# Kernel tuning notes

Hardware: AMD Instinct MI355X
Metric: run time of the kernel (lower is better)

## Reference

```python
import jax, jax.numpy as jnp
import numpy as np

NUM_STATES = 32768
NUM_LABELS = 64
BATCH = 512


def setup_inputs() -> dict:
    key = jax.random.key(0)
    k1, k2, k3, k4 = jax.random.split(key, 4)
    f = jax.random.normal(k1, (BATCH, NUM_LABELS), dtype=jnp.float32)
    # legal_state: binary indicator matrix [num_states, num_labels]
    S = jax.random.randint(k2, (NUM_STATES, NUM_LABELS), 0, 2).astype(jnp.float32)
    y = jax.random.uniform(k3, (BATCH, NUM_LABELS), dtype=jnp.float32)
    mask = jax.random.randint(k4, (BATCH, NUM_LABELS), 0, 2).astype(jnp.float32)
    return {"f": f, "S": S, "y": y, "mask": mask}


def reference(f, S, y, mask):
    # potential[s, b] = sum_i S[s, i] * f[b, i]
    potential = jnp.einsum('si,bi->sb', S, f)
    # stable softmax over the state axis (replaces exp/max/sum in original)
    P = jax.nn.softmax(potential, axis=0)  # [num_states, batch]
    # pMargin[b, i] = sum_{s: S[s,i]>0} P[s, b]  ->  indicator-matrix GEMM
    pMargin = jnp.einsum('sb,si->bi', P, S)  # [batch, num_labels]
    # per-column BCE (torch BCELoss clamps log at -100), masked, mean over batch
    logp = jnp.clip(jnp.log(pMargin), -100.0, None)
    log1mp = jnp.clip(jnp.log(1.0 - pMargin), -100.0, None)
    bce = -(y * logp + (1.0 - y) * log1mp) * mask  # [batch, num_labels]
    loss = jnp.sum(jnp.mean(bce, axis=0))  # sum over columns of per-column means
    return loss, pMargin
```

## Files before the change

kernel.cpp:

```cpp
#include <hip/hip_runtime.h>
#include <hip/hip_bf16.h>
#include <math.h>

#define N_STATES 32768
#define N_LABELS 64
#define N_BATCH  512

#define WS_M_F   0
#define ZP_F     1024
#define UP_F     65536
#define SB_BYTE  8650752u
#define STB_BYTE 12845056u

typedef __attribute__((ext_vector_type(8))) short          bfrag;
typedef __attribute__((ext_vector_type(4))) float          f32x4;
typedef __attribute__((ext_vector_type(8))) unsigned short u16x8;

static __device__ __forceinline__ unsigned short f2bf(float x) {
    __hip_bfloat16 h = __float2bfloat16(x);
    return *reinterpret_cast<unsigned short*>(&h);
}
static __device__ __forceinline__ float bf2f(unsigned short u) {
    __hip_bfloat16 h;
    *reinterpret_cast<unsigned short*>(&h) = u;
    return __bfloat162float(h);
}

typedef __attribute__((address_space(1))) const unsigned char g_u8;
typedef __attribute__((address_space(3))) unsigned char       l_u8;
static __device__ __forceinline__ void dma16(const void* g, void* l) {
    __builtin_amdgcn_global_load_lds((g_u8*)g, (l_u8*)l, 16, 0, 0);
}

__global__ __launch_bounds__(256) void prep_kernel(
    const float* __restrict__ f, const float* __restrict__ S,
    float* __restrict__ ws) {
    const int tb = blockIdx.x;
    const int t  = threadIdx.x;

    if (tb == 512) {
        for (int b = t; b < N_BATCH; b += 256) {
            const float* fr = f + b * N_LABELS;
            float m = 0.f;
            #pragma unroll
            for (int i = 0; i < N_LABELS; i++) m += fmaxf(fr[i], 0.f);
            ws[WS_M_F + b] = m;
        }
        return;
    }

    __shared__ alignas(16) unsigned short Sl[64 * 72];

    unsigned short* SbW = (unsigned short*)((char*)ws + SB_BYTE);
    unsigned short* StW = (unsigned short*)((char*)ws + STB_BYTE);

    const int r = t >> 2;
    const int q = t & 3;
    const int m = r & 7;

    const float4* p4 = reinterpret_cast<const float4*>(
        S + ((size_t)(tb * 64 + r)) * N_LABELS + q * 16);
    float4 v0 = p4[0], v1 = p4[1], v2 = p4[2], v3 = p4[3];
    float vf[16] = {v0.x,v0.y,v0.z,v0.w, v1.x,v1.y,v1.z,v1.w,
                    v2.x,v2.y,v2.z,v2.w, v3.x,v3.y,v3.z,v3.w};
    u16x8 lo8, hi8;
    #pragma unroll
    for (int j = 0; j < 8; j++) { lo8[j] = f2bf(vf[j]); hi8[j] = f2bf(vf[8 + j]); }

    *(u16x8*)&Sl[r * 72 + q * 16]     = lo8;
    *(u16x8*)&Sl[r * 72 + q * 16 + 8] = hi8;

    {
        unsigned short* dst = SbW + (size_t)tb * 4096 + r * 64 + (((2 * q) ^ (m & 6)) * 8);
        if (m & 1) { *(u16x8*)dst = hi8; *(u16x8*)(dst + 8) = lo8; }
        else       { *(u16x8*)dst = lo8; *(u16x8*)(dst + 8) = hi8; }
    }
    __syncthreads();

    const int i  = r;
    const int mi = i & 7;
    u16x8 tlo, thi;
    #pragma unroll
    for (int j = 0; j < 8; j++) {
        tlo[j] = Sl[(16 * q + j)     * 72 + i];
        thi[j] = Sl[(16 * q + 8 + j) * 72 + i];
    }
    {
        unsigned short* dst = StW + (size_t)tb * 4096 + i * 64 + (((2 * q) ^ (mi & 6)) * 8);
        if (mi & 1) { *(u16x8*)dst = thi; *(u16x8*)(dst + 8) = tlo; }
        else        { *(u16x8*)dst = tlo; *(u16x8*)(dst + 8) = thi; }
    }
}

__global__ __launch_bounds__(256, 2) void fused_kernel(
    const float* __restrict__ f, float* __restrict__ ws,
    float* __restrict__ out) {
    __shared__ alignas(16) unsigned short Sb2[2][4096];
    __shared__ alignas(16) unsigned short St2[2][4096];
    __shared__ alignas(16) unsigned short Et[64 * 72];

    const float* M = ws + WS_M_F;
    const char* SbG = (const char*)ws + SB_BYTE;
    const char* StG = (const char*)ws + STB_BYTE;

    const int t     = threadIdx.x;
    const int lane  = t & 63;
    const int w     = t >> 6;
    const int x     = lane & 15;
    const int quad  = lane >> 4;
    const int mm    = x & 7;
    const int btile = blockIdx.x >> 6;
    const int chunk = blockIdx.x & 63;
    const int tile0 = chunk * 8;

    bfrag fh[4][2], fl[4][2];
    #pragma unroll
    for (int nt = 0; nt < 4; nt++) {
        const float4* fp = reinterpret_cast<const float4*>(
            f + ((size_t)(btile * 64 + nt * 16 + x)) * N_LABELS);
        #pragma unroll
        for (int kh = 0; kh < 2; kh++) {
            float4 a = fp[kh * 8 + quad * 2];
            float4 b = fp[kh * 8 + quad * 2 + 1];
            float vv[8] = {a.x,a.y,a.z,a.w, b.x,b.y,b.z,b.w};
            #pragma unroll
            for (int j = 0; j < 8; j++) {
                unsigned short h = f2bf(vv[j]);
                fh[nt][kh][j] = (short)h;
                fl[nt][kh][j] = (short)f2bf(vv[j] - bf2f(h));
            }
        }
    }
    float Mv[4];
    #pragma unroll
    for (int nt = 0; nt < 4; nt++) Mv[nt] = M[btile * 64 + nt * 16 + x];

    f32x4 Uacc[4];
    #pragma unroll
    for (int nt = 0; nt < 4; nt++) Uacc[nt] = (f32x4){0.f, 0.f, 0.f, 0.f};
    float zacc[4] = {0.f, 0.f, 0.f, 0.f};

    auto stage = [&](int tile, int buf) {
        size_t gb = (size_t)tile * 8192 + (size_t)w * 2048 + (size_t)lane * 16;
        int lo = w * 2048;
        dma16(SbG + gb,        (char*)&Sb2[buf][0] + lo);
        dma16(SbG + gb + 1024, (char*)&Sb2[buf][0] + lo + 1024);
        dma16(StG + gb,        (char*)&St2[buf][0] + lo);
        dma16(StG + gb + 1024, (char*)&St2[buf][0] + lo + 1024);
    };

    stage(tile0 + 0, 0);
    stage(tile0 + 1, 1);
    asm volatile("s_waitcnt vmcnt(4)" ::: "memory");
    asm volatile("s_barrier" ::: "memory");

    #pragma unroll
    for (int st = 0; st < 8; st++) {
        const int cur = st & 1;
        const unsigned short* Sb = &Sb2[cur][0];
        const unsigned short* St = &St2[cur][0];

        bfrag a0 = *(const bfrag*)(Sb + (16 * w + x) * 64 + ((quad ^ mm) * 8));
        bfrag a1 = *(const bfrag*)(Sb + (16 * w + x) * 64 + (((quad + 4) ^ mm) * 8));
        #pragma unroll
        for (int nt = 0; nt < 4; nt++) {
            f32x4 acc = (f32x4){0.f, 0.f, 0.f, 0.f};
            acc = __builtin_amdgcn_mfma_f32_16x16x32_bf16(a0, fh[nt][0], acc, 0, 0, 0);
            acc = __builtin_amdgcn_mfma_f32_16x16x32_bf16(a1, fh[nt][1], acc, 0, 0, 0);
            acc = __builtin_amdgcn_mfma_f32_16x16x32_bf16(a0, fl[nt][0], acc, 0, 0, 0);
            acc = __builtin_amdgcn_mfma_f32_16x16x32_bf16(a1, fl[nt][1], acc, 0, 0, 0);
            float e0 = __expf(acc[0] - Mv[nt]);
            float e1 = __expf(acc[1] - Mv[nt]);
            float e2 = __expf(acc[2] - Mv[nt]);
            float e3 = __expf(acc[3] - Mv[nt]);
            zacc[nt] += (e0 + e1) + (e2 + e3);
            ushort4 ev;
            ev.x = f2bf(e0); ev.y = f2bf(e1); ev.z = f2bf(e2); ev.w = f2bf(e3);
            *(ushort4*)&Et[(nt * 16 + x) * 72 + 16 * w + quad * 4] = ev;
        }
        asm volatile("s_waitcnt lgkmcnt(0)" ::: "memory");
        asm volatile("s_barrier" ::: "memory");

        bfrag c0 = *(const bfrag*)(St + (16 * w + x) * 64 + ((quad ^ mm) * 8));
        bfrag c1 = *(const bfrag*)(St + (16 * w + x) * 64 + (((quad + 4) ^ mm) * 8));
        #pragma unroll
        for (int nt = 0; nt < 4; nt++) {
            bfrag e0 = *(const bfrag*)(Et + (nt * 16 + x) * 72 + quad * 8);
            bfrag e1 = *(const bfrag*)(Et + (nt * 16 + x) * 72 + 32 + quad * 8);
            Uacc[nt] = __builtin_amdgcn_mfma_f32_16x16x32_bf16(c0, e0, Uacc[nt], 0, 0, 0);
            Uacc[nt] = __builtin_amdgcn_mfma_f32_16x16x32_bf16(c1, e1, Uacc[nt], 0, 0, 0);
        }

        if (st < 6) {
            asm volatile("s_barrier" ::: "memory");
            stage(tile0 + st + 2, cur);
            asm volatile("s_waitcnt vmcnt(4)" ::: "memory");
            asm volatile("s_barrier" ::: "memory");
        } else if (st == 6) {
            asm volatile("s_waitcnt vmcnt(0)" ::: "memory");
            asm volatile("s_barrier" ::: "memory");
        }
    }

    float* Up = ws + UP_F;
    #pragma unroll
    for (int nt = 0; nt < 4; nt++) {
        #pragma unroll
        for (int r = 0; r < 4; r++) {
            int i = 16 * w + quad * 4 + r;
            Up[((btile * 64 + i) * 64 + chunk) * 64 + nt * 16 + x] = Uacc[nt][r];
        }
    }

    __syncthreads();
    float* zsh = (float*)Et;
    #pragma unroll
    for (int nt = 0; nt < 4; nt++) {
        float v = zacc[nt];
        v += __shfl_down(v, 32, 64);
        v += __shfl_down(v, 16, 64);
        if (quad == 0) zsh[w * 64 + nt * 16 + x] = v;
    }
    __syncthreads();
    if (t < 64) {
        float z = zsh[t] + zsh[64 + t] + zsh[128 + t] + zsh[192 + t];
        (ws + ZP_F)[(btile * 64 + chunk) * 64 + t] = z;
    }
    if (blockIdx.x == 0 && t == 0) out[0] = 0.f;
}

__global__ __launch_bounds__(256) void finalize_kernel(
    const float* __restrict__ ws, const float* __restrict__ y,
    const float* __restrict__ mask, float* __restrict__ out) {
    const int i     = blockIdx.x >> 1;
    const int b     = ((blockIdx.x & 1) << 8) + threadIdx.x;
    const int btile = b >> 6;
    const int bl    = b & 63;

    const float* zp = ws + ZP_F + (btile * 64) * 64 + bl;
    const float* up = ws + UP_F + ((btile * 64 + i) * 64) * 64 + bl;
    float z = 0.f, u = 0.f;
    #pragma unroll 8
    for (int c = 0; c < 64; c++) { z += zp[c * 64]; u += up[c * 64]; }

    float p = fminf(fmaxf(u / z, 0.f), 1.f);
    const int idx = b * 64 + i;
    out[1 + idx] = p;

    float lp  = fmaxf(logf(p), -100.f);
    float l1p = fmaxf(logf(1.f - p), -100.f);
    float yy = y[idx];
    float bce = -(yy * lp + (1.f - yy) * l1p) * mask[idx] * (1.f / (float)N_BATCH);

    float v = bce;
    #pragma unroll
    for (int off = 32; off > 0; off >>= 1) v += __shfl_down(v, off, 64);
    __shared__ float wsum[4];
    if ((threadIdx.x & 63) == 0) wsum[threadIdx.x >> 6] = v;
    __syncthreads();
    if (threadIdx.x == 0)
        atomicAdd(&out[0], wsum[0] + wsum[1] + wsum[2] + wsum[3]);
}

extern "C" void kernel_launch(void* const* d_in, const int* in_sizes, int n_in,
                              void* d_out, int out_size, void* d_ws, size_t ws_size,
                              hipStream_t stream) {
    const float* f    = (const float*)d_in[0];
    const float* S    = (const float*)d_in[1];
    const float* y    = (const float*)d_in[2];
    const float* mask = (const float*)d_in[3];
    float* out = (float*)d_out;
    float* ws  = (float*)d_ws;

    prep_kernel<<<513, 256, 0, stream>>>(f, S, ws);
    fused_kernel<<<512, 256, 0, stream>>>(f, ws, out);
    finalize_kernel<<<128, 256, 0, stream>>>(ws, y, mask, out);
}
```

Measured before the change: 96.55 us.

## Keep exp tile in registers for second GEMM and fold row-max into fused kernel

```diff
diff --git a/kernel.cpp b/kernel.cpp
--- a/kernel.cpp
+++ b/kernel.cpp
@@ -6,13 +6,13 @@
 #define N_LABELS 64
 #define N_BATCH  512
 
-#define WS_M_F   0
 #define ZP_F     1024
 #define UP_F     65536
 #define SB_BYTE  8650752u
 #define STB_BYTE 12845056u
 
 typedef __attribute__((ext_vector_type(8))) short          bfrag;
+typedef __attribute__((ext_vector_type(4))) short          bhalf;
 typedef __attribute__((ext_vector_type(4))) float          f32x4;
 typedef __attribute__((ext_vector_type(8))) unsigned short u16x8;
 
@@ -33,21 +33,9 @@
 }
 
 __global__ __launch_bounds__(256) void prep_kernel(
-    const float* __restrict__ f, const float* __restrict__ S,
-    float* __restrict__ ws) {
+    const float* __restrict__ S, float* __restrict__ ws) {
     const int tb = blockIdx.x;
     const int t  = threadIdx.x;
-
-    if (tb == 512) {
-        for (int b = t; b < N_BATCH; b += 256) {
-            const float* fr = f + b * N_LABELS;
-            float m = 0.f;
-            #pragma unroll
-            for (int i = 0; i < N_LABELS; i++) m += fmaxf(fr[i], 0.f);
-            ws[WS_M_F + b] = m;
-        }
-        return;
-    }
 
     __shared__ alignas(16) unsigned short Sl[64 * 72];
 
@@ -95,11 +83,8 @@
 __global__ __launch_bounds__(256, 2) void fused_kernel(
     const float* __restrict__ f, float* __restrict__ ws,
     float* __restrict__ out) {
-    __shared__ alignas(16) unsigned short Sb2[2][4096];
-    __shared__ alignas(16) unsigned short St2[2][4096];
-    __shared__ alignas(16) unsigned short Et[64 * 72];
-
-    const float* M = ws + WS_M_F;
+    __shared__ alignas(16) unsigned char smem[66560];
+
     const char* SbG = (const char*)ws + SB_BYTE;
     const char* StG = (const char*)ws + STB_BYTE;
 
@@ -114,10 +99,12 @@
     const int tile0 = chunk * 8;
 
     bfrag fh[4][2], fl[4][2];
+    float Mv[4];
     #pragma unroll
     for (int nt = 0; nt < 4; nt++) {
         const float4* fp = reinterpret_cast<const float4*>(
             f + ((size_t)(btile * 64 + nt * 16 + x)) * N_LABELS);
+        float msum = 0.f;
         #pragma unroll
         for (int kh = 0; kh < 2; kh++) {
             float4 a = fp[kh * 8 + quad * 2];
@@ -125,28 +112,29 @@
             float vv[8] = {a.x,a.y,a.z,a.w, b.x,b.y,b.z,b.w};
             #pragma unroll
             for (int j = 0; j < 8; j++) {
+                msum += fmaxf(vv[j], 0.f);
                 unsigned short h = f2bf(vv[j]);
                 fh[nt][kh][j] = (short)h;
                 fl[nt][kh][j] = (short)f2bf(vv[j] - bf2f(h));
             }
         }
-    }
-    float Mv[4];
-    #pragma unroll
-    for (int nt = 0; nt < 4; nt++) Mv[nt] = M[btile * 64 + nt * 16 + x];
-
-    f32x4 Uacc[4];
-    #pragma unroll
-    for (int nt = 0; nt < 4; nt++) Uacc[nt] = (f32x4){0.f, 0.f, 0.f, 0.f};
+        msum += __shfl_xor(msum, 16, 64);
+        msum += __shfl_xor(msum, 32, 64);
+        Mv[nt] = msum;
+    }
+
+    f32x4 Uacc[16];
+    #pragma unroll
+    for (int e = 0; e < 16; e++) Uacc[e] = (f32x4){0.f, 0.f, 0.f, 0.f};
     float zacc[4] = {0.f, 0.f, 0.f, 0.f};
 
     auto stage = [&](int tile, int buf) {
         size_t gb = (size_t)tile * 8192 + (size_t)w * 2048 + (size_t)lane * 16;
         int lo = w * 2048;
-        dma16(SbG + gb,        (char*)&Sb2[buf][0] + lo);
-        dma16(SbG + gb + 1024, (char*)&Sb2[buf][0] + lo + 1024);
-        dma16(StG + gb,        (char*)&St2[buf][0] + lo);
-        dma16(StG + gb + 1024, (char*)&St2[buf][0] + lo + 1024);
+        dma16(SbG + gb,        smem + buf * 8192 + lo);
+        dma16(SbG + gb + 1024, smem + buf * 8192 + lo + 1024);
+        dma16(StG + gb,        smem + 16384 + buf * 8192 + lo);
+        dma16(StG + gb + 1024, smem + 16384 + buf * 8192 + lo + 1024);
     };
 
     stage(tile0 + 0, 0);
@@ -157,11 +145,21 @@
     #pragma unroll
     for (int st = 0; st < 8; st++) {
         const int cur = st & 1;
-        const unsigned short* Sb = &Sb2[cur][0];
-        const unsigned short* St = &St2[cur][0];
+        const unsigned short* Sb = (const unsigned short*)(smem + cur * 8192);
+        const unsigned short* St = (const unsigned short*)(smem + 16384 + cur * 8192);
 
         bfrag a0 = *(const bfrag*)(Sb + (16 * w + x) * 64 + ((quad ^ mm) * 8));
         bfrag a1 = *(const bfrag*)(Sb + (16 * w + x) * 64 + (((quad + 4) ^ mm) * 8));
+
+        bfrag A8[4];
+        #pragma unroll
+        for (int it = 0; it < 4; it++) {
+            bhalf a4 = *(const bhalf*)(St + (16 * it + x) * 64 +
+                         (((2 * w + (quad >> 1)) ^ mm) * 8) + 4 * (quad & 1));
+            bfrag tmp = {a4[0], a4[1], a4[2], a4[3], 0, 0, 0, 0};
+            A8[it] = tmp;
+        }
+
         #pragma unroll
         for (int nt = 0; nt < 4; nt++) {
             f32x4 acc = (f32x4){0.f, 0.f, 0.f, 0.f};
@@ -174,21 +172,12 @@
             float e2 = __expf(acc[2] - Mv[nt]);
             float e3 = __expf(acc[3] - Mv[nt]);
             zacc[nt] += (e0 + e1) + (e2 + e3);
-            ushort4 ev;
-            ev.x = f2bf(e0); ev.y = f2bf(e1); ev.z = f2bf(e2); ev.w = f2bf(e3);
-            *(ushort4*)&Et[(nt * 16 + x) * 72 + 16 * w + quad * 4] = ev;
-        }
-        asm volatile("s_waitcnt lgkmcnt(0)" ::: "memory");
-        asm volatile("s_barrier" ::: "memory");
-
-        bfrag c0 = *(const bfrag*)(St + (16 * w + x) * 64 + ((quad ^ mm) * 8));
-        bfrag c1 = *(const bfrag*)(St + (16 * w + x) * 64 + (((quad + 4) ^ mm) * 8));
-        #pragma unroll
-        for (int nt = 0; nt < 4; nt++) {
-            bfrag e0 = *(const bfrag*)(Et + (nt * 16 + x) * 72 + quad * 8);
-            bfrag e1 = *(const bfrag*)(Et + (nt * 16 + x) * 72 + 32 + quad * 8);
-            Uacc[nt] = __builtin_amdgcn_mfma_f32_16x16x32_bf16(c0, e0, Uacc[nt], 0, 0, 0);
-            Uacc[nt] = __builtin_amdgcn_mfma_f32_16x16x32_bf16(c1, e1, Uacc[nt], 0, 0, 0);
+            bfrag Bf = {(short)f2bf(e0), (short)f2bf(e1),
+                        (short)f2bf(e2), (short)f2bf(e3), 0, 0, 0, 0};
+            #pragma unroll
+            for (int it = 0; it < 4; it++)
+                Uacc[it * 4 + nt] =
+                    __builtin_amdgcn_mfma_f32_16x16x32_bf16(A8[it], Bf, Uacc[it * 4 + nt], 0, 0, 0);
         }
 
         if (st < 6) {
@@ -202,18 +191,15 @@
         }
     }
 
-    float* Up = ws + UP_F;
-    #pragma unroll
-    for (int nt = 0; nt < 4; nt++) {
-        #pragma unroll
-        for (int r = 0; r < 4; r++) {
-            int i = 16 * w + quad * 4 + r;
-            Up[((btile * 64 + i) * 64 + chunk) * 64 + nt * 16 + x] = Uacc[nt][r];
-        }
-    }
-
-    __syncthreads();
-    float* zsh = (float*)Et;
+    __syncthreads();
+    float* mg  = (float*)smem;
+    float* zsh = (float*)(smem + 65536);
+    #pragma unroll
+    for (int e = 0; e < 16; e++) {
+        #pragma unroll
+        for (int r = 0; r < 4; r++)
+            mg[w * 4096 + (e * 4 + r) * 64 + lane] = Uacc[e][r];
+    }
     #pragma unroll
     for (int nt = 0; nt < 4; nt++) {
         float v = zacc[nt];
@@ -222,6 +208,19 @@
         if (quad == 0) zsh[w * 64 + nt * 16 + x] = v;
     }
     __syncthreads();
+
+    float* Up = ws + UP_F;
+    #pragma unroll
+    for (int k = 0; k < 16; k++) {
+        int idx = k * 256 + t;
+        int e  = idx >> 6;
+        int ln = idx & 63;
+        int it = e >> 4, nt = (e >> 2) & 3, r = e & 3;
+        int i  = it * 16 + (ln >> 4) * 4 + r;
+        int b  = nt * 16 + (ln & 15);
+        float s = mg[idx] + mg[4096 + idx] + mg[8192 + idx] + mg[12288 + idx];
+        Up[((btile * 64 + i) * 64 + chunk) * 64 + b] = s;
+    }
     if (t < 64) {
         float z = zsh[t] + zsh[64 + t] + zsh[128 + t] + zsh[192 + t];
         (ws + ZP_F)[(btile * 64 + chunk) * 64 + t] = z;
@@ -272,7 +271,7 @@
     float* out = (float*)d_out;
     float* ws  = (float*)d_ws;
 
-    prep_kernel<<<513, 256, 0, stream>>>(f, S, ws);
+    prep_kernel<<<512, 256, 0, stream>>>(S, ws);
     fused_kernel<<<512, 256, 0, stream>>>(f, ws, out);
     finalize_kernel<<<128, 256, 0, stream>>>(ws, y, mask, out);
 }
```

After: 94.79 us. No clear change (-1.8%).
